# Optimization experiments

Measured on AMD Instinct MI355X. Metric: run time of the kernel, lower is better.

The kernel has to match this reference:

```python
import jax, jax.numpy as jnp
import numpy as np

IN_DIM, HID, MEM, OUT = 512, 1024, 1024, 512
BATCH = 4096
HIST = 5  # hist_steps hard-coded in MMU.__init__

_LINEARS = [("inpgate", IN_DIM, HID), ("rec_inpgate", OUT, HID), ("mem_inpgate", MEM, HID),
            ("inp", IN_DIM, HID), ("rec_inp", OUT, HID),
            ("readgate", IN_DIM, MEM), ("rec_readgate", OUT, MEM), ("mem_readgate", MEM, MEM),
            ("decoder", HID, MEM),
            ("writegate", IN_DIM, MEM), ("rec_writegate", OUT, MEM), ("mem_writegate", MEM, MEM),
            ("encoder", MEM, HID)]


def setup_inputs() -> dict:
    key = jax.random.key(0)
    ks = iter(jax.random.split(key, 2 * len(_LINEARS) + 4))
    d = {"input": jax.random.normal(next(ks), (IN_DIM, BATCH), jnp.float32)}
    for name, fin, fout in _LINEARS:
        bound = 1.0 / np.sqrt(fin)  # torch nn.Linear default init range
        d["W_" + name] = jax.random.uniform(next(ks), (fout, fin), jnp.float32, -bound, bound)
        d["b_" + name] = jax.random.uniform(next(ks), (fout,), jnp.float32, -bound, bound)
    d["w_hid_out"] = jax.random.uniform(next(ks), (OUT, MEM), jnp.float32)  # torch.rand
    return d


def reference(input, W_inpgate, b_inpgate, W_rec_inpgate, b_rec_inpgate,
              W_mem_inpgate, b_mem_inpgate, W_inp, b_inp, W_rec_inp, b_rec_inp,
              W_readgate, b_readgate, W_rec_readgate, b_rec_readgate,
              W_mem_readgate, b_mem_readgate, W_decoder, b_decoder,
              W_writegate, b_writegate, W_rec_writegate, b_rec_writegate,
              W_mem_writegate, b_mem_writegate, W_encoder, b_encoder, w_hid_out):
    B = input.shape[1]
    lin = lambda x, W, b: x @ W.T + b
    # fresh module: history is zeros except last slot = current input (transposed to [B, in])
    xs = jnp.concatenate([jnp.zeros((HIST - 1, B, IN_DIM), input.dtype), input.T[None]], axis=0)

    def step(carry, x):
        out, mem = carry  # [B, OUT], [B, MEM]
        block_inp = jax.nn.sigmoid(lin(x, W_inp, b_inp) + lin(out, W_rec_inp, b_rec_inp))
        inp_gate = jax.nn.sigmoid(lin(x, W_inpgate, b_inpgate) + lin(mem, W_mem_inpgate, b_mem_inpgate)
                                  + lin(out, W_rec_inpgate, b_rec_inpgate))
        read_gate = jax.nn.sigmoid(lin(x, W_readgate, b_readgate) + lin(mem, W_mem_readgate, b_mem_readgate)
                                   + lin(out, W_rec_readgate, b_rec_readgate))
        decoded_mem = lin(read_gate * mem, W_decoder, b_decoder)
        hidden = decoded_mem + block_inp * inp_gate  # [B, HID] (HID == MEM)
        write_gate = jax.nn.sigmoid(lin(x, W_writegate, b_writegate) + lin(mem, W_mem_writegate, b_mem_writegate)
                                    + lin(out, W_rec_writegate, b_rec_writegate))
        encoded = jnp.tanh(lin(hidden, W_encoder, b_encoder))
        mem = (1.0 - write_gate) * mem + write_gate * encoded
        out = hidden @ w_hid_out.T  # w_hid_out.mm(hidden.T).T
        return (out, mem), None

    init = (jnp.zeros((B, OUT), input.dtype), jnp.zeros((B, MEM), input.dtype))
    (out, _mem), _ = jax.lax.scan(step, init, xs)
    return out
```

## Files before the change

kernel.cpp:

```cpp
#include <hip/hip_runtime.h>
#include <hip/hip_bf16.h>
#include <math.h>

typedef __hip_bfloat16 bf16;
typedef __attribute__((ext_vector_type(8))) short s16x8;
typedef __attribute__((ext_vector_type(4))) float f32x4;

__device__ __forceinline__ float fsig(float x) {
  return __builtin_amdgcn_rcpf(1.0f + __expf(-x));
}
__device__ __forceinline__ float ftanh(float x) { return 2.0f * fsig(2.0f * x) - 1.0f; }
__device__ __forceinline__ float dot4(float4 a, float4 b) {
  return a.x * b.x + a.y * b.y + a.z * b.z + a.w * b.w;
}
__device__ __forceinline__ float wred(float s) {
#pragma unroll
  for (int off = 32; off > 0; off >>= 1) s += __shfl_down(s, off, 64);
  return s;
}
__device__ __forceinline__ float b2f(unsigned short u) {
  return __uint_as_float((unsigned)u << 16);
}
__device__ __forceinline__ float4 b2f4(ushort4 u) {
  return make_float4(b2f(u.x), b2f(u.y), b2f(u.z), b2f(u.w));
}

#define WG7_STRIDE 5120

__global__ void setup(const float* __restrict__ W_inp, const float* __restrict__ W_ig,
                      const float* __restrict__ W_rg, const float* __restrict__ W_ho,
                      const float* __restrict__ W_dec, const float* __restrict__ W_enc,
                      const float* __restrict__ input,
                      const float* __restrict__ Wri, const float* __restrict__ Wmig,
                      const float* __restrict__ Wrig, const float* __restrict__ Wmrg,
                      const float* __restrict__ Wrrg, const float* __restrict__ Wmwg,
                      const float* __restrict__ Wrwg,
                      const float* __restrict__ b_inp, const float* __restrict__ b_rinp,
                      const float* __restrict__ b_ig, const float* __restrict__ b_mig,
                      const float* __restrict__ b_rig, const float* __restrict__ b_wg,
                      const float* __restrict__ b_mwg, const float* __restrict__ b_rwg,
                      const float* __restrict__ b_dec, const float* __restrict__ b_enc,
                      bf16* __restrict__ Wcat,
                      bf16* __restrict__ WhoB, bf16* __restrict__ Wcat2, bf16* __restrict__ Wdt,
                      bf16* __restrict__ WencB, bf16* __restrict__ Xb,
                      float* __restrict__ out_s, float* __restrict__ mem_s,
                      float* __restrict__ vout, float* __restrict__ Web,
                      bf16* __restrict__ Wg7) {
  __shared__ float t[32][33];
  const int id = blockIdx.x, tid = threadIdx.x;
  if (id < 12288) {
    const int i = id * 256 + tid;
    if (i < 524288) {
      Wcat[i] = __float2bfloat16(W_inp[i]);
    } else if (i < 1048576) {
      Wcat[i] = __float2bfloat16(W_ig[i - 524288]);
    } else if (i < 1572864) {
      Wcat[i] = __float2bfloat16(W_rg[i - 1048576]);
    } else if (i < 2097152) {
      const int k = i - 1572864;
      const bf16 vv = __float2bfloat16(W_ho[k]);
      WhoB[k] = vv;
      Wcat2[(size_t)(k >> 10) * 2048 + (k & 1023)] = vv;
    } else {
      const int k = i - 2097152;
      WencB[k] = __float2bfloat16(W_enc[k]);
    }
  } else if (id < 14336) {
    const int b = id - 12288;
    const int i0 = (b >> 7) * 32, b0 = (b & 127) * 32;
    const int tx = tid & 31, ty = tid >> 5;
#pragma unroll
    for (int r = ty; r < 32; r += 8) t[r][tx] = input[(size_t)(i0 + r) * 4096 + b0 + tx];
    __syncthreads();
#pragma unroll
    for (int r = ty; r < 32; r += 8)
      Xb[(size_t)(b0 + r) * 512 + i0 + tx] = __float2bfloat16(t[tx][r]);
  } else if (id < 15360) {
    const int b = id - 14336;
    const int j0 = (b >> 5) * 32, k0 = (b & 31) * 32;
    const int tx = tid & 31, ty = tid >> 5;
#pragma unroll
    for (int r = ty; r < 32; r += 8) t[r][tx] = W_dec[(size_t)(j0 + r) * 1024 + k0 + tx];
    __syncthreads();
#pragma unroll
    for (int r = ty; r < 32; r += 8)
      Wdt[(size_t)(k0 + r) * 1024 + j0 + tx] = __float2bfloat16(t[tx][r]);
  } else if (id < 16896) {
    const int o = id - 15360;
    const float* row = (o < 512) ? (W_ho + (size_t)o * 1024) : (W_enc + (size_t)(o - 512) * 1024);
    const float4 a = *(const float4*)(row + tid * 4);
    const float4 b = *(const float4*)(b_dec + tid * 4);
    float s = wred(dot4(a, b));
    if ((tid & 63) == 0) t[0][tid >> 6] = s;
    __syncthreads();
    if (tid == 0) {
      const float d = t[0][0] + t[0][1] + t[0][2] + t[0][3];
      if (o < 512) vout[o] = d;
      else Web[o - 512] = d;
    }
  } else if (id < 18432) {
    const int id2 = id - 16896;
    const float4 bd = *(const float4*)(b_dec + tid * 4);
    const float4 v1 = *(const float4*)(b_inp + tid * 4);
    const float4 v2 = *(const float4*)(b_rinp + tid * 4);
    const float4 v3 = *(const float4*)(b_ig + tid * 4);
    const float4 v4 = *(const float4*)(b_mig + tid * 4);
    const float4 v5 = *(const float4*)(b_rig + tid * 4);
    float4 hv;
    hv.x = bd.x + fsig(v1.x + v2.x) * fsig(v3.x + v4.x + v5.x);
    hv.y = bd.y + fsig(v1.y + v2.y) * fsig(v3.y + v4.y + v5.y);
    hv.z = bd.z + fsig(v1.z + v2.z) * fsig(v3.z + v4.z + v5.z);
    hv.w = bd.w + fsig(v1.w + v2.w) * fsig(v3.w + v4.w + v5.w);
    const float* row =
        (id2 < 1024) ? (W_enc + (size_t)id2 * 1024) : (W_ho + (size_t)(id2 - 1024) * 1024);
    float s = wred(dot4(*(const float4*)(row + tid * 4), hv));
    if ((tid & 63) == 0) t[0][tid >> 6] = s;
    __syncthreads();
    if (tid == 0) {
      const float d = t[0][0] + t[0][1] + t[0][2] + t[0][3];
      if (id2 < 1024) {
        const float wg = fsig(b_wg[id2] + b_mwg[id2] + b_rwg[id2]);
        mem_s[id2] = wg * ftanh(b_enc[id2] + d);
      } else {
        out_s[id2 - 1024] = d;
      }
    }
  } else {
    const int b = id - 18432;
    const int j = b / 5, f = b - j * 5;
    const int col = f * 1024 + tid * 4;
    const float* src;
    int c0, stride;
    if (col < 512)       { src = Wri;  c0 = col;        stride = 512; }
    else if (col < 1536) { src = Wmig; c0 = col - 512;  stride = 1024; }
    else if (col < 2048) { src = Wrig; c0 = col - 1536; stride = 512; }
    else if (col < 3072) { src = Wmrg; c0 = col - 2048; stride = 1024; }
    else if (col < 3584) { src = Wrrg; c0 = col - 3072; stride = 512; }
    else if (col < 4608) { src = Wmwg; c0 = col - 3584; stride = 1024; }
    else                 { src = Wrwg; c0 = col - 4608; stride = 512; }
    const float4 v = *(const float4*)(src + (size_t)j * stride + c0);
    ushort4 u;
    u.x = __bfloat16_as_ushort(__float2bfloat16(v.x));
    u.y = __bfloat16_as_ushort(__float2bfloat16(v.y));
    u.z = __bfloat16_as_ushort(__float2bfloat16(v.z));
    u.w = __bfloat16_as_ushort(__float2bfloat16(v.w));
    *(ushort4*)(Wg7 + (size_t)j * WG7_STRIDE + col) = u;
  }
}

__global__ __launch_bounds__(256) void gates_pe(
    const bf16* __restrict__ Wg7, const float* __restrict__ b_inp,
    const float* __restrict__ b_rinp, const float* __restrict__ b_ig,
    const float* __restrict__ b_mig, const float* __restrict__ b_rig,
    const float* __restrict__ b_rg, const float* __restrict__ b_mrg,
    const float* __restrict__ b_rrg, const float* __restrict__ b_wg,
    const float* __restrict__ b_mwg, const float* __restrict__ b_rwg,
    const float* __restrict__ out_s, const float* __restrict__ mem_s,
    float* __restrict__ rgm, float* __restrict__ h0v, float* __restrict__ wgv,
    const bf16* __restrict__ WhoB, const bf16* __restrict__ WencB,
    const bf16* __restrict__ Wdt, bf16* __restrict__ Wcat2, bf16* __restrict__ Eb,
    int pe_blocks) {
  __shared__ char smem[32768];
  const int tid = threadIdx.x;
  if ((int)blockIdx.x >= pe_blocks) {
    float(*red)[4] = (float(*)[4])smem;
    const int j = blockIdx.x - pe_blocks, lane = tid & 63, wave = tid >> 6;
    const float4 z = make_float4(0.f, 0.f, 0.f, 0.f);
    const float4 o4 = (tid < 128) ? *(const float4*)(out_s + tid * 4) : z;
    const float4 m4 = *(const float4*)(mem_s + tid * 4);
    const bf16* rowb = Wg7 + (size_t)j * WG7_STRIDE;
    float p[7];
    p[0] = (tid < 128) ? dot4(b2f4(*(const ushort4*)(rowb + tid * 4)), o4) : 0.f;
    p[1] = dot4(b2f4(*(const ushort4*)(rowb + 512 + tid * 4)), m4);
    p[2] = (tid < 128) ? dot4(b2f4(*(const ushort4*)(rowb + 1536 + tid * 4)), o4) : 0.f;
    p[3] = dot4(b2f4(*(const ushort4*)(rowb + 2048 + tid * 4)), m4);
    p[4] = (tid < 128) ? dot4(b2f4(*(const ushort4*)(rowb + 3072 + tid * 4)), o4) : 0.f;
    p[5] = dot4(b2f4(*(const ushort4*)(rowb + 3584 + tid * 4)), m4);
    p[6] = (tid < 128) ? dot4(b2f4(*(const ushort4*)(rowb + 4608 + tid * 4)), o4) : 0.f;
#pragma unroll
    for (int d = 0; d < 7; ++d) {
      float s = wred(p[d]);
      if (lane == 0) red[d][wave] = s;
    }
    __syncthreads();
    if (tid == 0) {
      float D[7];
#pragma unroll
      for (int d = 0; d < 7; ++d) D[d] = red[d][0] + red[d][1] + red[d][2] + red[d][3];
      const float abi = b_inp[j] + b_rinp[j] + D[0];
      const float aig = b_ig[j] + b_mig[j] + b_rig[j] + D[1] + D[2];
      const float arg = b_rg[j] + b_mrg[j] + b_rrg[j] + D[3] + D[4];
      const float awg = b_wg[j] + b_mwg[j] + b_rwg[j] + D[5] + D[6];
      rgm[j] = fsig(arg) * mem_s[j];
      h0v[j] = fsig(abi) * fsig(aig);
      wgv[j] = fsig(awg);
    }
    return;
  }
  const int bi = blockIdx.x;
  const bf16* Ag;
  bf16* Cg;
  int m0, n0, cstride;
  if (bi < 128) {
    Ag = WhoB; Cg = Wcat2 + 1024; cstride = 2048;
    m0 = (bi >> 4) * 64; n0 = (bi & 15) * 64;
  } else {
    const int b2 = bi - 128;
    Ag = WencB; Cg = Eb; cstride = 1024;
    m0 = (b2 >> 4) * 64; n0 = (b2 & 15) * 64;
  }
  const int wave = tid >> 6, lane = tid & 63;
  const int wm = wave >> 1, wn = wave & 1;
  f32x4 acc[2][2] = {};

  auto STAGE = [&](int kt, unsigned bofs) {
#pragma unroll
    for (int i = 0; i < 2; ++i) {
      const int ci = i * 256 + tid;
      const int row = ci >> 3, ck = (ci & 7) ^ (row & 7);
      const bf16* g = Ag + (size_t)(m0 + row) * 1024 + kt + ck * 8;
      const unsigned lofs =
          (unsigned)__builtin_amdgcn_readfirstlane(bofs + (i * 256 + wave * 64) * 16);
      __builtin_amdgcn_global_load_lds(
          (const __attribute__((address_space(1))) void*)g,
          (__attribute__((address_space(3))) void*)(smem + lofs), 16, 0, 0);
    }
#pragma unroll
    for (int i = 0; i < 2; ++i) {
      const int ci = i * 256 + tid;
      const int row = ci >> 3, ck = (ci & 7) ^ (row & 7);
      const bf16* g = Wdt + (size_t)(n0 + row) * 1024 + kt + ck * 8;
      const unsigned lofs =
          (unsigned)__builtin_amdgcn_readfirstlane(bofs + 8192 + (i * 256 + wave * 64) * 16);
      __builtin_amdgcn_global_load_lds(
          (const __attribute__((address_space(1))) void*)g,
          (__attribute__((address_space(3))) void*)(smem + lofs), 16, 0, 0);
    }
  };

  STAGE(0, 0);
  __syncthreads();
  unsigned cur = 0;
  for (int kt = 0; kt < 1024; kt += 64) {
    if (kt + 64 < 1024) STAGE(kt + 64, (cur ^ 1u) * 16384u);
#pragma unroll
    for (int ks = 0; ks < 2; ++ks) {
      const int ckk = ks * 4 + (lane >> 4);
      const unsigned cofs = cur * 16384u;
      s16x8 af[2];
#pragma unroll
      for (int i = 0; i < 2; ++i) {
        const int R = wm * 32 + i * 16 + (lane & 15);
        af[i] = *(const s16x8*)(smem + cofs + (R * 8 + (ckk ^ (R & 7))) * 16);
      }
#pragma unroll
      for (int j = 0; j < 2; ++j) {
        const int R = wn * 32 + j * 16 + (lane & 15);
        const s16x8 bfr = *(const s16x8*)(smem + cofs + 8192 + (R * 8 + (ckk ^ (R & 7))) * 16);
#pragma unroll
        for (int i = 0; i < 2; ++i)
          acc[i][j] = __builtin_amdgcn_mfma_f32_16x16x32_bf16(af[i], bfr, acc[i][j], 0, 0, 0);
      }
    }
    __syncthreads();
    cur ^= 1u;
  }
  const int mb = (lane >> 4) * 4, nb = lane & 15;
#pragma unroll
  for (int i = 0; i < 2; ++i) {
#pragma unroll
    for (int j = 0; j < 2; ++j) {
      const int col = n0 + wn * 32 + j * 16 + nb;
#pragma unroll
      for (int r = 0; r < 4; ++r) {
        const int rowg = m0 + wm * 32 + i * 16 + mb + r;
        Cg[(size_t)rowg * cstride + col] = __float2bfloat16(acc[i][j][r]);
      }
    }
  }
}

__global__ void step_fuse(const bf16* __restrict__ Eb, const bf16* __restrict__ WencB,
                          const bf16* __restrict__ Wcat2, const bf16* __restrict__ WhoB,
                          const float* __restrict__ b_enc, const float* __restrict__ Web,
                          const float* __restrict__ vout, const float* __restrict__ rgm,
                          const float* __restrict__ h0v, const float* __restrict__ wgv,
                          float* __restrict__ mem_s, float* __restrict__ out_s) {
  __shared__ float red[4];
  const int id = blockIdx.x, tid = threadIdx.x;
  const float4 r4 = *(const float4*)(rgm + tid * 4);
  const float4 h4 = *(const float4*)(h0v + tid * 4);
  const bf16* Ar = (id < 1024) ? (Eb + (size_t)id * 1024)
                               : (Wcat2 + (size_t)(id - 1024) * 2048 + 1024);
  const bf16* Br =
      (id < 1024) ? (WencB + (size_t)id * 1024) : (WhoB + (size_t)(id - 1024) * 1024);
  const float4 a4 = b2f4(*(const ushort4*)(Ar + tid * 4));
  const float4 b4 = b2f4(*(const ushort4*)(Br + tid * 4));
  const float s = wred(dot4(a4, r4) + dot4(b4, h4));
  if ((tid & 63) == 0) red[tid >> 6] = s;
  __syncthreads();
  if (tid == 0) {
    const float d = red[0] + red[1] + red[2] + red[3];
    if (id < 1024) {
      const float wg = wgv[id];
      mem_s[id] = (1.0f - wg) * mem_s[id] + wg * ftanh(b_enc[id] + Web[id] + d);
    } else {
      out_s[id - 1024] = vout[id - 1024] + d;
    }
  }
}

__global__ void final_consts(const bf16* __restrict__ Wg7, const float* __restrict__ b_inp,
                             const float* __restrict__ b_rinp, const float* __restrict__ b_ig,
                             const float* __restrict__ b_mig, const float* __restrict__ b_rig,
                             const float* __restrict__ b_rg, const float* __restrict__ b_mrg,
                             const float* __restrict__ b_rrg, const float* __restrict__ out_s,
                             const float* __restrict__ mem_s, float* __restrict__ ccat) {
  __shared__ float red[5][4];
  const int id = blockIdx.x, tid = threadIdx.x, lane = tid & 63, wave = tid >> 6;
  const float4 z = make_float4(0.f, 0.f, 0.f, 0.f);
  const float4 o4 = (tid < 128) ? *(const float4*)(out_s + tid * 4) : z;
  const float4 m4 = *(const float4*)(mem_s + tid * 4);
  const bf16* rowb = Wg7 + (size_t)id * WG7_STRIDE;
  float p[5];
  p[0] = (tid < 128) ? dot4(b2f4(*(const ushort4*)(rowb + tid * 4)), o4) : 0.f;
  p[1] = dot4(b2f4(*(const ushort4*)(rowb + 512 + tid * 4)), m4);
  p[2] = (tid < 128) ? dot4(b2f4(*(const ushort4*)(rowb + 1536 + tid * 4)), o4) : 0.f;
  p[3] = dot4(b2f4(*(const ushort4*)(rowb + 2048 + tid * 4)), m4);
  p[4] = (tid < 128) ? dot4(b2f4(*(const ushort4*)(rowb + 3072 + tid * 4)), o4) : 0.f;
#pragma unroll
  for (int d = 0; d < 5; ++d) {
    float s = wred(p[d]);
    if (lane == 0) red[d][wave] = s;
  }
  __syncthreads();
  if (tid == 0) {
    float D[5];
#pragma unroll
    for (int d = 0; d < 5; ++d) D[d] = red[d][0] + red[d][1] + red[d][2] + red[d][3];
    ccat[id] = b_inp[id] + b_rinp[id] + D[0];
    ccat[1024 + id] = b_ig[id] + b_mig[id] + b_rig[id] + D[1] + D[2];
    ccat[2048 + id] = b_rg[id] + b_mrg[id] + b_rrg[id] + D[3] + D[4];
  }
}

__global__ __launch_bounds__(256, 4) void gemm_gates(const bf16* __restrict__ A,
                                                     const bf16* __restrict__ Wcat,
                                                     const float* __restrict__ ccat,
                                                     const float* __restrict__ mem_s,
                                                     bf16* __restrict__ Hcat) {
  __shared__ char smem[32768];
  const int tid = threadIdx.x, wave = tid >> 6, lane = tid & 63;
  const int wm = wave >> 1, wn = wave & 1;
  const int swz = (blockIdx.x & 7) * 128 + (blockIdx.x >> 3);
  const int m0 = (swz >> 4) * 64, n0 = (swz & 15) * 64;
  f32x4 acc[3][2][2] = {};

  for (int kt = 0; kt < 512; kt += 64) {
    __syncthreads();
#pragma unroll
    for (int i = 0; i < 2; ++i) {
      const int ci = i * 256 + tid;
      const int row = ci >> 3, ck = (ci & 7) ^ (row & 7);
      const bf16* g = A + (size_t)(m0 + row) * 512 + kt + ck * 8;
      const unsigned lofs = (unsigned)__builtin_amdgcn_readfirstlane((i * 256 + wave * 64) * 16);
      __builtin_amdgcn_global_load_lds(
          (const __attribute__((address_space(1))) void*)g,
          (__attribute__((address_space(3))) void*)(smem + lofs), 16, 0, 0);
    }
#pragma unroll
    for (int gI = 0; gI < 3; ++gI) {
      const bf16* Bp = Wcat + gI * 524288;
#pragma unroll
      for (int i = 0; i < 2; ++i) {
        const int ci = i * 256 + tid;
        const int row = ci >> 3, ck = (ci & 7) ^ (row & 7);
        const bf16* g = Bp + (size_t)(n0 + row) * 512 + kt + ck * 8;
        const unsigned lofs = (unsigned)__builtin_amdgcn_readfirstlane(
            8192 + gI * 8192 + (i * 256 + wave * 64) * 16);
        __builtin_amdgcn_global_load_lds(
            (const __attribute__((address_space(1))) void*)g,
            (__attribute__((address_space(3))) void*)(smem + lofs), 16, 0, 0);
      }
    }
    __syncthreads();

#pragma unroll
    for (int ks = 0; ks < 2; ++ks) {
      const int ckk = ks * 4 + (lane >> 4);
      s16x8 af[2];
#pragma unroll
      for (int i = 0; i < 2; ++i) {
        const int R = wm * 32 + i * 16 + (lane & 15);
        af[i] = *(const s16x8*)(smem + (R * 8 + (ckk ^ (R & 7))) * 16);
      }
#pragma unroll
      for (int gI = 0; gI < 3; ++gI) {
#pragma unroll
        for (int j = 0; j < 2; ++j) {
          const int R = wn * 32 + j * 16 + (lane & 15);
          const s16x8 bfr =
              *(const s16x8*)(smem + 8192 + gI * 8192 + (R * 8 + (ckk ^ (R & 7))) * 16);
#pragma unroll
          for (int i = 0; i < 2; ++i)
            acc[gI][i][j] =
                __builtin_amdgcn_mfma_f32_16x16x32_bf16(af[i], bfr, acc[gI][i][j], 0, 0, 0);
        }
      }
    }
  }

  __syncthreads();
  bf16* sm = (bf16*)smem;
  bf16* sr = (bf16*)smem + 5120;
  const int mb = (lane >> 4) * 4, nb = lane & 15;
#pragma unroll
  for (int i = 0; i < 2; ++i) {
#pragma unroll
    for (int j = 0; j < 2; ++j) {
      const int colL = wn * 32 + j * 16 + nb;
      const int jg = n0 + colL;
      const float c0 = ccat[jg], c1 = ccat[1024 + jg], c2 = ccat[2048 + jg];
      const float m3 = mem_s[jg];
#pragma unroll
      for (int r = 0; r < 4; ++r) {
        const int rowL = wm * 32 + i * 16 + mb + r;
        const float h = fsig(acc[0][i][j][r] + c0) * fsig(acc[1][i][j][r] + c1);
        const float rg = fsig(acc[2][i][j][r] + c2) * m3;
        sm[rowL * 80 + colL] = __float2bfloat16(h);
        sr[rowL * 80 + colL] = __float2bfloat16(rg);
      }
    }
  }
  __syncthreads();
#pragma unroll
  for (int pp = 0; pp < 2; ++pp) {
    const int c = pp * 256 + tid;
    const int row = c >> 3, cc = c & 7;
    const s16x8 v0 = *(const s16x8*)(sm + row * 80 + cc * 8);
    const s16x8 v1 = *(const s16x8*)(sr + row * 80 + cc * 8);
    *(s16x8*)(Hcat + (size_t)(m0 + row) * 2048 + n0 + cc * 8) = v0;
    *(s16x8*)(Hcat + (size_t)(m0 + row) * 2048 + 1024 + n0 + cc * 8) = v1;
  }
}

__global__ __launch_bounds__(256, 4) void gemm_out(const bf16* __restrict__ A,
                                                   const bf16* __restrict__ Bp,
                                                   const float* __restrict__ vout,
                                                   float* __restrict__ outF) {
  __shared__ char smem[32768];
  const int tid = threadIdx.x, wave = tid >> 6, lane = tid & 63;
  const int wm = wave >> 1, wn = wave & 1;
  const int swz = (blockIdx.x & 7) * 64 + (blockIdx.x >> 3);
  const int m0 = (swz >> 3) * 64, n0 = (swz & 7) * 64;
  f32x4 acc[2][2] = {};

  auto STAGE = [&](int kt, unsigned bofs) {
#pragma unroll
    for (int i = 0; i < 2; ++i) {
      const int ci = i * 256 + tid;
      const int row = ci >> 3, ck = (ci & 7) ^ (row & 7);
      const bf16* g = A + (size_t)(m0 + row) * 2048 + kt + ck * 8;
      const unsigned lofs =
          (unsigned)__builtin_amdgcn_readfirstlane(bofs + (i * 256 + wave * 64) * 16);
      __builtin_amdgcn_global_load_lds(
          (const __attribute__((address_space(1))) void*)g,
          (__attribute__((address_space(3))) void*)(smem + lofs), 16, 0, 0);
    }
#pragma unroll
    for (int i = 0; i < 2; ++i) {
      const int ci = i * 256 + tid;
      const int row = ci >> 3, ck = (ci & 7) ^ (row & 7);
      const bf16* g = Bp + (size_t)(n0 + row) * 2048 + kt + ck * 8;
      const unsigned lofs =
          (unsigned)__builtin_amdgcn_readfirstlane(bofs + 8192 + (i * 256 + wave * 64) * 16);
      __builtin_amdgcn_global_load_lds(
          (const __attribute__((address_space(1))) void*)g,
          (__attribute__((address_space(3))) void*)(smem + lofs), 16, 0, 0);
    }
  };

  STAGE(0, 0);
  __syncthreads();
  unsigned cur = 0;
  for (int kt = 0; kt < 2048; kt += 64) {
    if (kt + 64 < 2048) STAGE(kt + 64, (cur ^ 1u) * 16384u);
#pragma unroll
    for (int ks = 0; ks < 2; ++ks) {
      const int ckk = ks * 4 + (lane >> 4);
      const unsigned cofs = cur * 16384u;
      s16x8 af[2];
#pragma unroll
      for (int i = 0; i < 2; ++i) {
        const int R = wm * 32 + i * 16 + (lane & 15);
        af[i] = *(const s16x8*)(smem + cofs + (R * 8 + (ckk ^ (R & 7))) * 16);
      }
#pragma unroll
      for (int j = 0; j < 2; ++j) {
        const int R = wn * 32 + j * 16 + (lane & 15);
        const s16x8 bfr = *(const s16x8*)(smem + cofs + 8192 + (R * 8 + (ckk ^ (R & 7))) * 16);
#pragma unroll
        for (int i = 0; i < 2; ++i)
          acc[i][j] = __builtin_amdgcn_mfma_f32_16x16x32_bf16(af[i], bfr, acc[i][j], 0, 0, 0);
      }
    }
    __syncthreads();
    cur ^= 1u;
  }

  const int mb = (lane >> 4) * 4, nb = lane & 15;
#pragma unroll
  for (int i = 0; i < 2; ++i) {
#pragma unroll
    for (int j = 0; j < 2; ++j) {
      const int col = n0 + wn * 32 + j * 16 + nb;
#pragma unroll
      for (int r = 0; r < 4; ++r) {
        const int rowg = m0 + wm * 32 + i * 16 + mb + r;
        outF[(size_t)rowg * 512 + col] = acc[i][j][r] + vout[col];
      }
    }
  }
}

extern "C" void kernel_launch(void* const* d_in, const int* in_sizes, int n_in, void* d_out,
                              int out_size, void* d_ws, size_t ws_size, hipStream_t stream) {
  const float* input  = (const float*)d_in[0];
  const float* W_ig   = (const float*)d_in[1];  const float* b_ig   = (const float*)d_in[2];
  const float* W_rig  = (const float*)d_in[3];  const float* b_rig  = (const float*)d_in[4];
  const float* W_mig  = (const float*)d_in[5];  const float* b_mig  = (const float*)d_in[6];
  const float* W_inp  = (const float*)d_in[7];  const float* b_inp  = (const float*)d_in[8];
  const float* W_rinp = (const float*)d_in[9];  const float* b_rinp = (const float*)d_in[10];
  const float* W_rg   = (const float*)d_in[11]; const float* b_rg   = (const float*)d_in[12];
  const float* W_rrg  = (const float*)d_in[13]; const float* b_rrg  = (const float*)d_in[14];
  const float* W_mrg  = (const float*)d_in[15]; const float* b_mrg  = (const float*)d_in[16];
  const float* W_dec  = (const float*)d_in[17]; const float* b_dec  = (const float*)d_in[18];
  const float* W_wg   = (const float*)d_in[19]; const float* b_wg   = (const float*)d_in[20];
  const float* W_rwg  = (const float*)d_in[21]; const float* b_rwg  = (const float*)d_in[22];
  const float* W_mwg  = (const float*)d_in[23]; const float* b_mwg  = (const float*)d_in[24];
  const float* W_enc  = (const float*)d_in[25]; const float* b_enc  = (const float*)d_in[26];
  const float* W_ho   = (const float*)d_in[27];
  (void)W_wg;

  char* ws = (char*)d_ws;
  float* out_s = (float*)(ws + 0);
  float* mem_s = (float*)(ws + 4096);
  float* rgm   = (float*)(ws + 8192);
  float* h0v   = (float*)(ws + 12288);
  float* wgv   = (float*)(ws + 16384);
  float* ccat  = (float*)(ws + 24576);
  float* vout  = (float*)(ws + 40960);
  float* Web   = (float*)(ws + 45056);
  bf16* Xb     = (bf16*)(ws + 2162688);
  bf16* Wcat   = (bf16*)(ws + 6356992);
  bf16* WhoB   = (bf16*)(ws + 9502720);
  bf16* Wcat2  = (bf16*)(ws + 10551296);
  bf16* Wdt    = (bf16*)(ws + 12648448);
  bf16* Hcat   = (bf16*)(ws + 14745600);
  bf16* Eb     = (bf16*)(ws + 31522816);
  bf16* WencB  = (bf16*)(ws + 35717120);
  bf16* Wg7    = (bf16*)(ws + 37814272);

  setup<<<23552, 256, 0, stream>>>(W_inp, W_ig, W_rg, W_ho, W_dec, W_enc, input,
                                   W_rinp, W_mig, W_rig, W_mrg, W_rrg, W_mwg, W_rwg,
                                   b_inp, b_rinp, b_ig, b_mig, b_rig, b_wg, b_mwg, b_rwg,
                                   b_dec, b_enc, Wcat, WhoB, Wcat2, Wdt, WencB, Xb,
                                   out_s, mem_s, vout, Web, Wg7);

  for (int s = 0; s < 3; ++s) {
    const int pe = (s == 0) ? 384 : 0;
    gates_pe<<<1024 + pe, 256, 0, stream>>>(Wg7, b_inp, b_rinp, b_ig, b_mig, b_rig, b_rg, b_mrg,
                                            b_rrg, b_wg, b_mwg, b_rwg, out_s, mem_s, rgm, h0v,
                                            wgv, WhoB, WencB, Wdt, Wcat2, Eb, pe);
    step_fuse<<<1536, 256, 0, stream>>>(Eb, WencB, Wcat2, WhoB, b_enc, Web, vout, rgm, h0v,
                                        wgv, mem_s, out_s);
  }

  final_consts<<<1024, 256, 0, stream>>>(Wg7, b_inp, b_rinp, b_ig, b_mig, b_rig, b_rg, b_mrg,
                                         b_rrg, out_s, mem_s, ccat);

  gemm_gates<<<1024, 256, 0, stream>>>(Xb, Wcat, ccat, mem_s, Hcat);

  gemm_out<<<512, 256, 0, stream>>>(Hcat, Wcat2, vout, (float*)d_out);
}
```

Before: 216.5 us.

## Move weight/input conversions into recurrent-step launches and interleave matrix layouts

The bf16 conversions of the input transpose and the W_inp/W_ig/W_rg concat move out of the setup kernel and into extra rider blocks of the second and third gates_pe launches. There they run alongside the small gate-matvec blocks, which do not fill the GPU on their own. W_ho and W_enc are stored only once, in interleaved 2048-wide buffers whose right half holds the products, so step_fuse reads one contiguous 16-byte row segment per thread. The vout/Web and out_s/mem_s setup reductions are merged into one block that reads each weight row once. The risk is extra branching in gates_pe and the rider work adding to the critical path of the sequential steps.

```diff
diff --git a/kernel.cpp b/kernel.cpp
--- a/kernel.cpp
+++ b/kernel.cpp
@@ -24,13 +24,25 @@
 __device__ __forceinline__ float4 b2f4(ushort4 u) {
   return make_float4(b2f(u.x), b2f(u.y), b2f(u.z), b2f(u.w));
 }
+__device__ __forceinline__ float dot8(s16x8 v, float4 a, float4 b) {
+  return b2f((unsigned short)v[0]) * a.x + b2f((unsigned short)v[1]) * a.y +
+         b2f((unsigned short)v[2]) * a.z + b2f((unsigned short)v[3]) * a.w +
+         b2f((unsigned short)v[4]) * b.x + b2f((unsigned short)v[5]) * b.y +
+         b2f((unsigned short)v[6]) * b.z + b2f((unsigned short)v[7]) * b.w;
+}
+__device__ __forceinline__ ushort4 f4tob4(float4 v) {
+  ushort4 u;
+  u.x = __bfloat16_as_ushort(__float2bfloat16(v.x));
+  u.y = __bfloat16_as_ushort(__float2bfloat16(v.y));
+  u.z = __bfloat16_as_ushort(__float2bfloat16(v.z));
+  u.w = __bfloat16_as_ushort(__float2bfloat16(v.w));
+  return u;
+}
 
 #define WG7_STRIDE 5120
 
-__global__ void setup(const float* __restrict__ W_inp, const float* __restrict__ W_ig,
-                      const float* __restrict__ W_rg, const float* __restrict__ W_ho,
-                      const float* __restrict__ W_dec, const float* __restrict__ W_enc,
-                      const float* __restrict__ input,
+__global__ void setup(const float* __restrict__ W_ho, const float* __restrict__ W_dec,
+                      const float* __restrict__ W_enc,
                       const float* __restrict__ Wri, const float* __restrict__ Wmig,
                       const float* __restrict__ Wrig, const float* __restrict__ Wmrg,
                       const float* __restrict__ Wrrg, const float* __restrict__ Wmwg,
@@ -40,43 +52,25 @@
                       const float* __restrict__ b_rig, const float* __restrict__ b_wg,
                       const float* __restrict__ b_mwg, const float* __restrict__ b_rwg,
                       const float* __restrict__ b_dec, const float* __restrict__ b_enc,
-                      bf16* __restrict__ Wcat,
-                      bf16* __restrict__ WhoB, bf16* __restrict__ Wcat2, bf16* __restrict__ Wdt,
-                      bf16* __restrict__ WencB, bf16* __restrict__ Xb,
+                      bf16* __restrict__ Wcat2, bf16* __restrict__ Wdt,
+                      bf16* __restrict__ EW2,
                       float* __restrict__ out_s, float* __restrict__ mem_s,
                       float* __restrict__ vout, float* __restrict__ Web,
                       bf16* __restrict__ Wg7) {
   __shared__ float t[32][33];
   const int id = blockIdx.x, tid = threadIdx.x;
-  if (id < 12288) {
-    const int i = id * 256 + tid;
-    if (i < 524288) {
-      Wcat[i] = __float2bfloat16(W_inp[i]);
-    } else if (i < 1048576) {
-      Wcat[i] = __float2bfloat16(W_ig[i - 524288]);
-    } else if (i < 1572864) {
-      Wcat[i] = __float2bfloat16(W_rg[i - 1048576]);
-    } else if (i < 2097152) {
-      const int k = i - 1572864;
-      const bf16 vv = __float2bfloat16(W_ho[k]);
-      WhoB[k] = vv;
-      Wcat2[(size_t)(k >> 10) * 2048 + (k & 1023)] = vv;
+  if (id < 1536) {
+    const int elem = (id * 256 + tid) * 4;
+    if (elem < 524288) {
+      const float4 v = *(const float4*)(W_ho + elem);
+      *(ushort4*)(Wcat2 + (size_t)(elem >> 10) * 2048 + (elem & 1023)) = f4tob4(v);
     } else {
-      const int k = i - 2097152;
-      WencB[k] = __float2bfloat16(W_enc[k]);
-    }
-  } else if (id < 14336) {
-    const int b = id - 12288;
-    const int i0 = (b >> 7) * 32, b0 = (b & 127) * 32;
-    const int tx = tid & 31, ty = tid >> 5;
-#pragma unroll
-    for (int r = ty; r < 32; r += 8) t[r][tx] = input[(size_t)(i0 + r) * 4096 + b0 + tx];
-    __syncthreads();
-#pragma unroll
-    for (int r = ty; r < 32; r += 8)
-      Xb[(size_t)(b0 + r) * 512 + i0 + tx] = __float2bfloat16(t[tx][r]);
-  } else if (id < 15360) {
-    const int b = id - 14336;
+      const int k = elem - 524288;
+      const float4 v = *(const float4*)(W_enc + k);
+      *(ushort4*)(EW2 + (size_t)(k >> 10) * 2048 + (k & 1023)) = f4tob4(v);
+    }
+  } else if (id < 2560) {
+    const int b = id - 1536;
     const int j0 = (b >> 5) * 32, k0 = (b & 31) * 32;
     const int tx = tid & 31, ty = tid >> 5;
 #pragma unroll
@@ -85,21 +79,8 @@
 #pragma unroll
     for (int r = ty; r < 32; r += 8)
       Wdt[(size_t)(k0 + r) * 1024 + j0 + tx] = __float2bfloat16(t[tx][r]);
-  } else if (id < 16896) {
-    const int o = id - 15360;
-    const float* row = (o < 512) ? (W_ho + (size_t)o * 1024) : (W_enc + (size_t)(o - 512) * 1024);
-    const float4 a = *(const float4*)(row + tid * 4);
-    const float4 b = *(const float4*)(b_dec + tid * 4);
-    float s = wred(dot4(a, b));
-    if ((tid & 63) == 0) t[0][tid >> 6] = s;
-    __syncthreads();
-    if (tid == 0) {
-      const float d = t[0][0] + t[0][1] + t[0][2] + t[0][3];
-      if (o < 512) vout[o] = d;
-      else Web[o - 512] = d;
-    }
-  } else if (id < 18432) {
-    const int id2 = id - 16896;
+  } else if (id < 4096) {
+    const int o = id - 2560;
     const float4 bd = *(const float4*)(b_dec + tid * 4);
     const float4 v1 = *(const float4*)(b_inp + tid * 4);
     const float4 v2 = *(const float4*)(b_rinp + tid * 4);
@@ -112,21 +93,30 @@
     hv.z = bd.z + fsig(v1.z + v2.z) * fsig(v3.z + v4.z + v5.z);
     hv.w = bd.w + fsig(v1.w + v2.w) * fsig(v3.w + v4.w + v5.w);
     const float* row =
-        (id2 < 1024) ? (W_enc + (size_t)id2 * 1024) : (W_ho + (size_t)(id2 - 1024) * 1024);
-    float s = wred(dot4(*(const float4*)(row + tid * 4), hv));
-    if ((tid & 63) == 0) t[0][tid >> 6] = s;
+        (o < 512) ? (W_ho + (size_t)o * 1024) : (W_enc + (size_t)(o - 512) * 1024);
+    const float4 a = *(const float4*)(row + tid * 4);
+    const float s1 = wred(dot4(a, bd));
+    const float s2 = wred(dot4(a, hv));
+    if ((tid & 63) == 0) {
+      t[0][tid >> 6] = s1;
+      t[1][tid >> 6] = s2;
+    }
     __syncthreads();
     if (tid == 0) {
-      const float d = t[0][0] + t[0][1] + t[0][2] + t[0][3];
-      if (id2 < 1024) {
-        const float wg = fsig(b_wg[id2] + b_mwg[id2] + b_rwg[id2]);
-        mem_s[id2] = wg * ftanh(b_enc[id2] + d);
+      const float d1 = t[0][0] + t[0][1] + t[0][2] + t[0][3];
+      const float d2 = t[1][0] + t[1][1] + t[1][2] + t[1][3];
+      if (o < 512) {
+        vout[o] = d1;
+        out_s[o] = d2;
       } else {
-        out_s[id2 - 1024] = d;
+        const int e = o - 512;
+        Web[e] = d1;
+        const float wg = fsig(b_wg[e] + b_mwg[e] + b_rwg[e]);
+        mem_s[e] = wg * ftanh(b_enc[e] + d2);
       }
     }
   } else {
-    const int b = id - 18432;
+    const int b = id - 4096;
     const int j = b / 5, f = b - j * 5;
     const int col = f * 1024 + tid * 4;
     const float* src;
@@ -139,12 +129,7 @@
     else if (col < 4608) { src = Wmwg; c0 = col - 3584; stride = 1024; }
     else                 { src = Wrwg; c0 = col - 4608; stride = 512; }
     const float4 v = *(const float4*)(src + (size_t)j * stride + c0);
-    ushort4 u;
-    u.x = __bfloat16_as_ushort(__float2bfloat16(v.x));
-    u.y = __bfloat16_as_ushort(__float2bfloat16(v.y));
-    u.z = __bfloat16_as_ushort(__float2bfloat16(v.z));
-    u.w = __bfloat16_as_ushort(__float2bfloat16(v.w));
-    *(ushort4*)(Wg7 + (size_t)j * WG7_STRIDE + col) = u;
+    *(ushort4*)(Wg7 + (size_t)j * WG7_STRIDE + col) = f4tob4(v);
   }
 }
 
@@ -157,14 +142,16 @@
     const float* __restrict__ b_mwg, const float* __restrict__ b_rwg,
     const float* __restrict__ out_s, const float* __restrict__ mem_s,
     float* __restrict__ rgm, float* __restrict__ h0v, float* __restrict__ wgv,
-    const bf16* __restrict__ WhoB, const bf16* __restrict__ WencB,
-    const bf16* __restrict__ Wdt, bf16* __restrict__ Wcat2, bf16* __restrict__ Eb,
-    int pe_blocks) {
+    const bf16* __restrict__ Wdt, bf16* __restrict__ Wcat2, bf16* __restrict__ EW2,
+    const float* __restrict__ input, bf16* __restrict__ Xb,
+    const float* __restrict__ W_inp, const float* __restrict__ W_ig,
+    const float* __restrict__ W_rg, bf16* __restrict__ Wcat,
+    int riders, int mode) {
   __shared__ char smem[32768];
   const int tid = threadIdx.x;
-  if ((int)blockIdx.x >= pe_blocks) {
+  if ((int)blockIdx.x >= riders) {
     float(*red)[4] = (float(*)[4])smem;
-    const int j = blockIdx.x - pe_blocks, lane = tid & 63, wave = tid >> 6;
+    const int j = blockIdx.x - riders, lane = tid & 63, wave = tid >> 6;
     const float4 z = make_float4(0.f, 0.f, 0.f, 0.f);
     const float4 o4 = (tid < 128) ? *(const float4*)(out_s + tid * 4) : z;
     const float4 m4 = *(const float4*)(mem_s + tid * 4);
@@ -197,16 +184,38 @@
     }
     return;
   }
+  if (mode == 1) {
+    float(*t)[33] = (float(*)[33])smem;
+    const int b = blockIdx.x;
+    const int i0 = (b >> 7) * 32, b0 = (b & 127) * 32;
+    const int tx = tid & 31, ty = tid >> 5;
+#pragma unroll
+    for (int r = ty; r < 32; r += 8) t[r][tx] = input[(size_t)(i0 + r) * 4096 + b0 + tx];
+    __syncthreads();
+#pragma unroll
+    for (int r = ty; r < 32; r += 8)
+      Xb[(size_t)(b0 + r) * 512 + i0 + tx] = __float2bfloat16(t[tx][r]);
+    return;
+  }
+  if (mode == 2) {
+    const int elem = ((int)blockIdx.x * 256 + tid) * 4;
+    float4 v;
+    if (elem < 524288) v = *(const float4*)(W_inp + elem);
+    else if (elem < 1048576) v = *(const float4*)(W_ig + elem - 524288);
+    else v = *(const float4*)(W_rg + elem - 1048576);
+    *(ushort4*)(Wcat + elem) = f4tob4(v);
+    return;
+  }
   const int bi = blockIdx.x;
   const bf16* Ag;
   bf16* Cg;
-  int m0, n0, cstride;
+  int m0, n0;
   if (bi < 128) {
-    Ag = WhoB; Cg = Wcat2 + 1024; cstride = 2048;
+    Ag = Wcat2; Cg = Wcat2 + 1024;
     m0 = (bi >> 4) * 64; n0 = (bi & 15) * 64;
   } else {
     const int b2 = bi - 128;
-    Ag = WencB; Cg = Eb; cstride = 1024;
+    Ag = EW2; Cg = EW2 + 1024;
     m0 = (b2 >> 4) * 64; n0 = (b2 & 15) * 64;
   }
   const int wave = tid >> 6, lane = tid & 63;
@@ -218,7 +227,7 @@
     for (int i = 0; i < 2; ++i) {
       const int ci = i * 256 + tid;
       const int row = ci >> 3, ck = (ci & 7) ^ (row & 7);
-      const bf16* g = Ag + (size_t)(m0 + row) * 1024 + kt + ck * 8;
+      const bf16* g = Ag + (size_t)(m0 + row) * 2048 + kt + ck * 8;
       const unsigned lofs =
           (unsigned)__builtin_amdgcn_readfirstlane(bofs + (i * 256 + wave * 64) * 16);
       __builtin_amdgcn_global_load_lds(
@@ -274,29 +283,27 @@
 #pragma unroll
       for (int r = 0; r < 4; ++r) {
         const int rowg = m0 + wm * 32 + i * 16 + mb + r;
-        Cg[(size_t)rowg * cstride + col] = __float2bfloat16(acc[i][j][r]);
-      }
-    }
-  }
-}
-
-__global__ void step_fuse(const bf16* __restrict__ Eb, const bf16* __restrict__ WencB,
-                          const bf16* __restrict__ Wcat2, const bf16* __restrict__ WhoB,
+        Cg[(size_t)rowg * 2048 + col] = __float2bfloat16(acc[i][j][r]);
+      }
+    }
+  }
+}
+
+__global__ void step_fuse(const bf16* __restrict__ EW2, const bf16* __restrict__ Wcat2,
                           const float* __restrict__ b_enc, const float* __restrict__ Web,
                           const float* __restrict__ vout, const float* __restrict__ rgm,
                           const float* __restrict__ h0v, const float* __restrict__ wgv,
                           float* __restrict__ mem_s, float* __restrict__ out_s) {
   __shared__ float red[4];
   const int id = blockIdx.x, tid = threadIdx.x;
-  const float4 r4 = *(const float4*)(rgm + tid * 4);
-  const float4 h4 = *(const float4*)(h0v + tid * 4);
-  const bf16* Ar = (id < 1024) ? (Eb + (size_t)id * 1024)
-                               : (Wcat2 + (size_t)(id - 1024) * 2048 + 1024);
-  const bf16* Br =
-      (id < 1024) ? (WencB + (size_t)id * 1024) : (WhoB + (size_t)(id - 1024) * 1024);
-  const float4 a4 = b2f4(*(const ushort4*)(Ar + tid * 4));
-  const float4 b4 = b2f4(*(const ushort4*)(Br + tid * 4));
-  const float s = wred(dot4(a4, r4) + dot4(b4, h4));
+  const bf16* row =
+      (id < 1024) ? (EW2 + (size_t)id * 2048) : (Wcat2 + (size_t)(id - 1024) * 2048);
+  const s16x8 v = *(const s16x8*)(row + tid * 8);
+  const int c = (tid * 8) & 1023;
+  const float* vec = (tid < 128) ? h0v : rgm;
+  const float4 x0 = *(const float4*)(vec + c);
+  const float4 x1 = *(const float4*)(vec + c + 4);
+  const float s = wred(dot8(v, x0, x1));
   if ((tid & 63) == 0) red[tid >> 6] = s;
   __syncthreads();
   if (tid == 0) {
@@ -553,27 +560,26 @@
   float* Web   = (float*)(ws + 45056);
   bf16* Xb     = (bf16*)(ws + 2162688);
   bf16* Wcat   = (bf16*)(ws + 6356992);
-  bf16* WhoB   = (bf16*)(ws + 9502720);
   bf16* Wcat2  = (bf16*)(ws + 10551296);
   bf16* Wdt    = (bf16*)(ws + 12648448);
   bf16* Hcat   = (bf16*)(ws + 14745600);
-  bf16* Eb     = (bf16*)(ws + 31522816);
-  bf16* WencB  = (bf16*)(ws + 35717120);
+  bf16* EW2    = (bf16*)(ws + 31522816);
   bf16* Wg7    = (bf16*)(ws + 37814272);
 
-  setup<<<23552, 256, 0, stream>>>(W_inp, W_ig, W_rg, W_ho, W_dec, W_enc, input,
-                                   W_rinp, W_mig, W_rig, W_mrg, W_rrg, W_mwg, W_rwg,
-                                   b_inp, b_rinp, b_ig, b_mig, b_rig, b_wg, b_mwg, b_rwg,
-                                   b_dec, b_enc, Wcat, WhoB, Wcat2, Wdt, WencB, Xb,
-                                   out_s, mem_s, vout, Web, Wg7);
+  setup<<<9216, 256, 0, stream>>>(W_ho, W_dec, W_enc,
+                                  W_rinp, W_mig, W_rig, W_mrg, W_rrg, W_mwg, W_rwg,
+                                  b_inp, b_rinp, b_ig, b_mig, b_rig, b_wg, b_mwg, b_rwg,
+                                  b_dec, b_enc, Wcat2, Wdt, EW2, out_s, mem_s, vout, Web, Wg7);
 
   for (int s = 0; s < 3; ++s) {
-    const int pe = (s == 0) ? 384 : 0;
-    gates_pe<<<1024 + pe, 256, 0, stream>>>(Wg7, b_inp, b_rinp, b_ig, b_mig, b_rig, b_rg, b_mrg,
-                                            b_rrg, b_wg, b_mwg, b_rwg, out_s, mem_s, rgm, h0v,
-                                            wgv, WhoB, WencB, Wdt, Wcat2, Eb, pe);
-    step_fuse<<<1536, 256, 0, stream>>>(Eb, WencB, Wcat2, WhoB, b_enc, Web, vout, rgm, h0v,
-                                        wgv, mem_s, out_s);
+    const int riders = (s == 0) ? 384 : (s == 1) ? 2048 : 1536;
+    const int mode = s;
+    gates_pe<<<1024 + riders, 256, 0, stream>>>(
+        Wg7, b_inp, b_rinp, b_ig, b_mig, b_rig, b_rg, b_mrg, b_rrg, b_wg, b_mwg, b_rwg,
+        out_s, mem_s, rgm, h0v, wgv, Wdt, Wcat2, EW2, input, Xb, W_inp, W_ig, W_rg, Wcat,
+        riders, mode);
+    step_fuse<<<1536, 256, 0, stream>>>(EW2, Wcat2, b_enc, Web, vout, rgm, h0v, wgv, mem_s,
+                                        out_s);
   }
 
   final_consts<<<1024, 256, 0, stream>>>(Wg7, b_inp, b_rinp, b_ig, b_mig, b_rig, b_rg, b_mrg,
```

New measurement: 213.5 us, median of 2. Within noise of the previous version (-1.4%).
